# Performance work log

Measured on AMD Instinct MI355X. Metric: run time of the kernel, lower is better.

## Reference

```python
import jax, jax.numpy as jnp
import numpy as np

NEG_SLOPE = 0.2  # PyG GATv2Conv default negative_slope


def _gatv2(h, src, dst, Wl, bl, Wr, br, att, bias, N):
    """GATv2Conv (concat=True). h: [N,Fin]; att: [H,F]; returns [N,H*F]."""
    H, F = att.shape
    xl = (h @ Wl + bl).reshape(N, H, F)  # source transform
    xr = (h @ Wr + br).reshape(N, H, F)  # target transform
    # per-edge GATv2 score: a^T LeakyReLU(xl[src] + xr[dst])
    e = jax.nn.leaky_relu(xl[src] + xr[dst], negative_slope=NEG_SLOPE)  # [E,H,F]
    logits = jnp.einsum('ehf,hf->eh', e, att)  # [E,H]
    # segment softmax over destination nodes (self-loops guarantee nonempty segments)
    m = jax.ops.segment_max(logits, dst, num_segments=N)  # [N,H]
    p = jnp.exp(logits - m[dst])
    s = jax.ops.segment_sum(p, dst, num_segments=N)  # [N,H]
    alpha = p / s[dst]  # [E,H]
    out = jax.ops.segment_sum(alpha[:, :, None] * xl[src], dst, num_segments=N)  # [N,H,F]
    return out.reshape(N, H * F) + bias


def setup_inputs() -> dict:
    key = jax.random.key(0)
    ks = jax.random.split(key, 16)
    N, E = 30000, 480000
    L, D, H, F = 50, 100, 3, 100
    W = D * H  # 300
    sc = 0.1  # keep activations stable through 5 layers
    return {
        'x': jax.random.randint(ks[0], (N,), 0, L),
        'edge_index': jax.random.randint(ks[1], (2, E), 0, N),
        'emb': jax.random.normal(ks[2], (L, D), jnp.float32),
        'Wl0': jax.random.normal(ks[3], (D, W), jnp.float32) * sc,
        'bl0': jnp.zeros((W,), jnp.float32),
        'Wr0': jax.random.normal(ks[4], (D, W), jnp.float32) * sc,
        'br0': jnp.zeros((W,), jnp.float32),
        'att0': jax.random.normal(ks[5], (H, F), jnp.float32) * sc,
        'bias0': jnp.zeros((W,), jnp.float32),
        'Wl': jax.random.normal(ks[6], (4, W, W), jnp.float32) * sc,
        'bl': jnp.zeros((4, W), jnp.float32),
        'Wr': jax.random.normal(ks[7], (4, W, W), jnp.float32) * sc,
        'br': jnp.zeros((4, W), jnp.float32),
        'att': jax.random.normal(ks[8], (4, H, F), jnp.float32) * sc,
        'bias': jnp.zeros((4, W), jnp.float32),
    }


def reference(x, edge_index, emb, Wl0, bl0, Wr0, br0, att0, bias0,
              Wl, bl, Wr, br, att, bias):
    N = x.shape[0]
    loops = jnp.arange(N)
    src = jnp.concatenate([edge_index[0], loops])  # PyG add_self_loops=True
    dst = jnp.concatenate([edge_index[1], loops])
    h = emb[x]  # node_embedding(x).squeeze()
    h = jax.nn.relu(_gatv2(h, src, dst, Wl0, bl0, Wr0, br0, att0, bias0, N))
    for i in range(4):  # remaining num_gnn_layers-1 convs, each followed by ReLU
        h = jax.nn.relu(_gatv2(h, src, dst, Wl[i], bl[i], Wr[i], br[i], att[i], bias[i], N))
    return h  # [N, heads*hidden] = [N, 300]
```

## Files before the change

### kernel.cpp

```cpp
#include <hip/hip_runtime.h>

#define NODES   30000
#define E0N     480000
#define ETOT    510000
#define D0      100
#define WDIM    300
#define NW      600
#define NEG     0.2f

typedef __bf16 bf16x8 __attribute__((ext_vector_type(8)));
typedef float  f32x4  __attribute__((ext_vector_type(4)));

__global__ void gather_emb(const int* __restrict__ x, const float* __restrict__ emb,
                           float* __restrict__ h, int n, int d) {
    int t = blockIdx.x * 256 + threadIdx.x;
    if (t >= n * d) return;
    int i = t / d, k = t - i * d;
    h[t] = emb[x[i] * d + k];
}

__global__ void count_edges(const int* __restrict__ ei, int* __restrict__ counts) {
    int e = blockIdx.x * 256 + threadIdx.x;
    if (e >= ETOT) return;
    int d = (e < E0N) ? ei[E0N + e] : (e - E0N);
    atomicAdd(&counts[d], 1);
}

__global__ __launch_bounds__(1024) void scan_kernel(const int* __restrict__ counts,
                                                    int* __restrict__ offsets, int n) {
    __shared__ int lds[1024];
    const int CH = 32;
    int t = threadIdx.x;
    int base = t * CH;
    int loc[CH];
    int sum = 0;
    #pragma unroll
    for (int i = 0; i < CH; i++) {
        int v = (base + i < n) ? counts[base + i] : 0;
        loc[i] = sum;
        sum += v;
    }
    lds[t] = sum;
    __syncthreads();
    for (int off = 1; off < 1024; off <<= 1) {
        int v = (t >= off) ? lds[t - off] : 0;
        __syncthreads();
        lds[t] += v;
        __syncthreads();
    }
    int ex = (t == 0) ? 0 : lds[t - 1];
    #pragma unroll
    for (int i = 0; i < CH; i++) {
        int idx = base + i;
        if (idx < n) offsets[idx] = ex + loc[i];
    }
    if (t == 0) offsets[n] = lds[1023];
}

__global__ void scatter_edges(const int* __restrict__ ei, const int* __restrict__ offsets,
                              int* __restrict__ cursor, int* __restrict__ csr_src) {
    int e = blockIdx.x * 256 + threadIdx.x;
    if (e >= ETOT) return;
    int s, d;
    if (e < E0N) { s = ei[e]; d = ei[E0N + e]; }
    else         { s = e - E0N; d = s; }
    int pos = offsets[d] + atomicAdd(&cursor[d], 1);
    csr_src[pos] = s;
}

__global__ void make_bfrag(const float* __restrict__ Bl, const float* __restrict__ Br,
                           bf16x8* __restrict__ out, int K, int ksteps) {
    int t = blockIdx.x * 256 + threadIdx.x;
    int total = ksteps * 40 * 64;
    if (t >= total) return;
    int lane = t & 63;
    int n16  = (t >> 6) % 40;
    int s    = t / (64 * 40);
    int c = n16 * 16 + (lane & 15);
    union { bf16x8 v; __bf16 e[8]; } hi, lo;
    #pragma unroll
    for (int j = 0; j < 8; j++) {
        int k = s * 32 + ((lane >> 4) * 8) + j;
        float x = 0.f;
        if (k < K && c < NW)
            x = (c < WDIM) ? Bl[(size_t)k * WDIM + c] : Br[(size_t)k * WDIM + c - WDIM];
        __bf16 h = (__bf16)x;
        hi.e[j] = h;
        lo.e[j] = (__bf16)(x - (float)h);
    }
    size_t base = ((size_t)(s * 40 + n16) * 2) * 64 + lane;
    out[base]      = hi.v;
    out[base + 64] = lo.v;
}

__global__ __launch_bounds__(256) void gemm_mfma(
    const float* __restrict__ A, const bf16x8* __restrict__ Bfrag,
    const float* __restrict__ bl, const float* __restrict__ br,
    float* __restrict__ Cl, float* __restrict__ Cr,
    int M, int K, int ksteps) {

    __shared__ bf16x8 Alds[8][2][64];
    __shared__ bf16x8 Blds[8][2][64];

    int id = blockIdx.x;
    int mb = (id & 7) + 8 * (id / 40);
    int cb = (id >> 3) % 5;
    if (mb >= 235) return;

    int tid  = threadIdx.x;
    int lane = tid & 63;
    int wid  = tid >> 6;
    int wm = wid >> 1, wn = wid & 1;
    int row0 = mb * 128;

    f32x4 acc[4][4] = {};

    for (int s = 0; s < ksteps; s++) {
        int kt = s * 32;
        #pragma unroll
        for (int u0 = 0; u0 < 2; u0++) {
            int u = u0 * 256 + tid;
            int m16  = u >> 6;
            int slot = u & 63;
            int kh = slot >> 4, rl = slot & 15;
            int gr = row0 + m16 * 16 + rl;
            int gc = kt + kh * 8;
            float4 v0 = make_float4(0.f,0.f,0.f,0.f), v1 = v0;
            if (gr < M) {
                const float* ap = A + (size_t)gr * K + gc;
                if (gc + 4 <= K) v0 = *(const float4*)ap;
                if (gc + 8 <= K) v1 = *(const float4*)(ap + 4);
            }
            union { bf16x8 v; __bf16 e[8]; } hi, lo;
            const float* xs0 = (const float*)&v0;
            const float* xs1 = (const float*)&v1;
            #pragma unroll
            for (int j = 0; j < 8; j++) {
                float x = (j < 4) ? xs0[j] : xs1[j - 4];
                __bf16 h = (__bf16)x;
                hi.e[j] = h;
                lo.e[j] = (__bf16)(x - (float)h);
            }
            Alds[m16][0][slot] = hi.v;
            Alds[m16][1][slot] = lo.v;
        }
        {
            const float4* bsrc = (const float4*)(Bfrag + ((size_t)(s * 40 + cb * 8) * 2) * 64);
            float4* bdst = (float4*)&Blds[0][0][0];
            #pragma unroll
            for (int c = 0; c < 4; c++)
                bdst[c * 256 + tid] = bsrc[c * 256 + tid];
        }
        __syncthreads();

        bf16x8 af[4][2], bfr[4][2];
        #pragma unroll
        for (int m = 0; m < 4; m++) {
            af[m][0] = Alds[wm * 4 + m][0][lane];
            af[m][1] = Alds[wm * 4 + m][1][lane];
        }
        #pragma unroll
        for (int n = 0; n < 4; n++) {
            bfr[n][0] = Blds[wn * 4 + n][0][lane];
            bfr[n][1] = Blds[wn * 4 + n][1][lane];
        }
        #pragma unroll
        for (int m = 0; m < 4; m++)
            #pragma unroll
            for (int n = 0; n < 4; n++) {
                acc[m][n] = __builtin_amdgcn_mfma_f32_16x16x32_bf16(af[m][1], bfr[n][1], acc[m][n], 0, 0, 0);
                acc[m][n] = __builtin_amdgcn_mfma_f32_16x16x32_bf16(af[m][1], bfr[n][0], acc[m][n], 0, 0, 0);
                acc[m][n] = __builtin_amdgcn_mfma_f32_16x16x32_bf16(af[m][0], bfr[n][1], acc[m][n], 0, 0, 0);
                acc[m][n] = __builtin_amdgcn_mfma_f32_16x16x32_bf16(af[m][0], bfr[n][0], acc[m][n], 0, 0, 0);
            }
        __syncthreads();
    }

    int r0 = row0 + wm * 64;
    int c0 = cb * 128 + wn * 64;
    #pragma unroll
    for (int m = 0; m < 4; m++)
        #pragma unroll
        for (int n = 0; n < 4; n++) {
            #pragma unroll
            for (int reg = 0; reg < 4; reg++) {
                int gr = r0 + m * 16 + (lane >> 4) * 4 + reg;
                int gc = c0 + n * 16 + (lane & 15);
                if (gr < M && gc < NW) {
                    bool left = gc < WDIM;
                    int cc = left ? gc : gc - WDIM;
                    float v = acc[m][n][reg] + (left ? bl[cc] : br[cc]);
                    (left ? Cl : Cr)[(size_t)gr * WDIM + cc] = v;
                }
            }
        }
}

__global__ __launch_bounds__(256) void gat_edge_agg(
    const float* __restrict__ xl, const float* __restrict__ xr,
    const int* __restrict__ offsets, const int* __restrict__ csr_src,
    const float* __restrict__ att, const float* __restrict__ bias,
    float* __restrict__ hout) {
    int node = (blockIdx.x * 256 + threadIdx.x) >> 6;
    int lane = threadIdx.x & 63;
    if (node >= NODES) return;

    float aw[5], xrv[5];
    #pragma unroll
    for (int j = 0; j < 5; j++) {
        int f = lane + 64 * j;
        aw[j]  = (f < WDIM) ? att[f] : 0.f;
        xrv[j] = xr[(size_t)node * WDIM + ((f < WDIM) ? f : 0)];
    }

    float m0 = -1e38f, m1 = -1e38f, m2 = -1e38f;
    float s0 = 0.f, s1 = 0.f, s2 = 0.f;
    float acc[5] = {};

    int beg = offsets[node], end = offsets[node + 1];
    for (int i = beg; i < end; i += 2) {
        bool act_b = (i + 1) < end;
        int sa = csr_src[i];
        int sb = csr_src[act_b ? i + 1 : i];
        const float* ra = xl + (size_t)sa * WDIM;
        const float* rb = xl + (size_t)sb * WDIM;
        float va[5], vb[5];
        #pragma unroll
        for (int j = 0; j < 5; j++) {
            va[j] = ra[lane + 64 * j];
            vb[j] = rb[lane + 64 * j];
        }
        float pa0 = 0.f, pa1 = 0.f, pa2 = 0.f;
        float pb0 = 0.f, pb1 = 0.f, pb2 = 0.f;
        #pragma unroll
        for (int j = 0; j < 5; j++) {
            int f = lane + 64 * j;
            float ta = va[j] + xrv[j]; ta = fmaxf(ta, NEG * ta);
            float tb = vb[j] + xrv[j]; tb = fmaxf(tb, NEG * tb);
            float qa = ta * aw[j], qb = tb * aw[j];
            if (j == 0)      { pa0 += qa; pb0 += qb; }
            else if (j == 2) { pa1 += qa; pb1 += qb; }
            else if (j == 4) { pa2 += qa; pb2 += qb; }
            else if (j == 1) {
                if (f < 100) { pa0 += qa; pb0 += qb; } else { pa1 += qa; pb1 += qb; }
            } else {
                if (f < 200) { pa1 += qa; pb1 += qb; } else { pa2 += qa; pb2 += qb; }
            }
        }
        pa0 += __shfl_xor(pa0, 1, 64); pa1 += __shfl_xor(pa1, 1, 64); pa2 += __shfl_xor(pa2, 1, 64);
        pb0 += __shfl_xor(pb0, 1, 64); pb1 += __shfl_xor(pb1, 1, 64); pb2 += __shfl_xor(pb2, 1, 64);
        pa0 += __shfl_xor(pa0, 2, 64); pa1 += __shfl_xor(pa1, 2, 64); pa2 += __shfl_xor(pa2, 2, 64);
        pb0 += __shfl_xor(pb0, 2, 64); pb1 += __shfl_xor(pb1, 2, 64); pb2 += __shfl_xor(pb2, 2, 64);
        int r = lane & 3;
        float qa = (r == 1) ? pa1 : ((r == 2) ? pa2 : pa0);
        float qb = (r == 1) ? pb1 : ((r == 2) ? pb2 : pb0);
        qa += __shfl_xor(qa, 4, 64);  qb += __shfl_xor(qb, 4, 64);
        qa += __shfl_xor(qa, 8, 64);  qb += __shfl_xor(qb, 8, 64);
        qa += __shfl_xor(qa, 16, 64); qb += __shfl_xor(qb, 16, 64);
        qa += __shfl_xor(qa, 32, 64); qb += __shfl_xor(qb, 32, 64);
        pa0 = __shfl(qa, 0, 64); pa1 = __shfl(qa, 1, 64); pa2 = __shfl(qa, 2, 64);
        pb0 = __shfl(qb, 0, 64); pb1 = __shfl(qb, 1, 64); pb2 = __shfl(qb, 2, 64);
        if (!act_b) { pb0 = -3e38f; pb1 = -3e38f; pb2 = -3e38f; }

        float hi0 = fmaxf(pa0, pb0), hi1 = fmaxf(pa1, pb1), hi2 = fmaxf(pa2, pb2);
        if (hi0 > m0 + 8.f || hi1 > m1 + 8.f || hi2 > m2 + 8.f) {
            float nm0 = fmaxf(m0, hi0), nm1 = fmaxf(m1, hi1), nm2 = fmaxf(m2, hi2);
            float e0 = __expf(m0 - nm0), e1 = __expf(m1 - nm1), e2 = __expf(m2 - nm2);
            s0 *= e0; s1 *= e1; s2 *= e2;
            #pragma unroll
            for (int j = 0; j < 5; j++) {
                int f = lane + 64 * j;
                float e = (j == 0) ? e0 : (j == 2) ? e1 : (j == 4) ? e2 :
                          (j == 1) ? ((f < 100) ? e0 : e1) : ((f < 200) ? e1 : e2);
                acc[j] *= e;
            }
            m0 = nm0; m1 = nm1; m2 = nm2;
        }
        float ca0 = __expf(pa0 - m0), ca1 = __expf(pa1 - m1), ca2 = __expf(pa2 - m2);
        float cb0 = __expf(pb0 - m0), cb1 = __expf(pb1 - m1), cb2 = __expf(pb2 - m2);
        s0 += ca0 + cb0; s1 += ca1 + cb1; s2 += ca2 + cb2;
        #pragma unroll
        for (int j = 0; j < 5; j++) {
            int f = lane + 64 * j;
            float ca = (j == 0) ? ca0 : (j == 2) ? ca1 : (j == 4) ? ca2 :
                       (j == 1) ? ((f < 100) ? ca0 : ca1) : ((f < 200) ? ca1 : ca2);
            float cb = (j == 0) ? cb0 : (j == 2) ? cb1 : (j == 4) ? cb2 :
                       (j == 1) ? ((f < 100) ? cb0 : cb1) : ((f < 200) ? cb1 : cb2);
            acc[j] = fmaf(ca, va[j], acc[j]);
            acc[j] = fmaf(cb, vb[j], acc[j]);
        }
    }

    float i0 = 1.f / s0, i1 = 1.f / s1, i2 = 1.f / s2;
    #pragma unroll
    for (int j = 0; j < 5; j++) {
        int f = lane + 64 * j;
        if (f < WDIM) {
            float is = (j == 0) ? i0 : (j == 2) ? i1 : (j == 4) ? i2 :
                       (j == 1) ? ((f < 100) ? i0 : i1) : ((f < 200) ? i1 : i2);
            float o = acc[j] * is + bias[f];
            hout[(size_t)node * WDIM + f] = fmaxf(o, 0.f);
        }
    }
}

static inline size_t align256(size_t x) { return (x + 255) & ~(size_t)255; }

extern "C" void kernel_launch(void* const* d_in, const int* in_sizes, int n_in,
                              void* d_out, int out_size, void* d_ws, size_t ws_size,
                              hipStream_t stream) {
    const int*   x     = (const int*)d_in[0];
    const int*   ei    = (const int*)d_in[1];
    const float* emb   = (const float*)d_in[2];
    const float* Wl0   = (const float*)d_in[3];
    const float* bl0   = (const float*)d_in[4];
    const float* Wr0   = (const float*)d_in[5];
    const float* br0   = (const float*)d_in[6];
    const float* att0  = (const float*)d_in[7];
    const float* bias0 = (const float*)d_in[8];
    const float* Wl    = (const float*)d_in[9];
    const float* bl    = (const float*)d_in[10];
    const float* Wr    = (const float*)d_in[11];
    const float* br    = (const float*)d_in[12];
    const float* att   = (const float*)d_in[13];
    const float* bias  = (const float*)d_in[14];

    char* ws = (char*)d_ws;
    size_t off = 0;
    float* h      = (float*)(ws + off); off = align256(off + (size_t)NODES * WDIM * 4);
    float* xlb    = (float*)(ws + off); off = align256(off + (size_t)NODES * WDIM * 4);
    float* xrb    = (float*)(ws + off); off = align256(off + (size_t)NODES * WDIM * 4);
    int* counts   = (int*)(ws + off);   off = align256(off + (size_t)NODES * 4);
    int* cursor   = (int*)(ws + off);   off = align256(off + (size_t)NODES * 4);
    int* offsets  = (int*)(ws + off);   off = align256(off + (size_t)(NODES + 1) * 4);
    int* csr_src  = (int*)(ws + off);   off = align256(off + (size_t)ETOT * 4);
    bf16x8* bfrag = (bf16x8*)(ws + off); off = align256(off + (size_t)10 * 40 * 2 * 64 * 16);

    float* out = (float*)d_out;

    hipMemsetAsync(counts, 0, (size_t)NODES * 4, stream);
    hipMemsetAsync(cursor, 0, (size_t)NODES * 4, stream);
    count_edges<<<(ETOT + 255) / 256, 256, 0, stream>>>(ei, counts);
    scan_kernel<<<1, 1024, 0, stream>>>(counts, offsets, NODES);
    scatter_edges<<<(ETOT + 255) / 256, 256, 0, stream>>>(ei, offsets, cursor, csr_src);

    gather_emb<<<(NODES * D0 + 255) / 256, 256, 0, stream>>>(x, emb, h, NODES, D0);

    int agg_blocks = (NODES + 3) / 4;

    {
        int ks = 4;
        int bf_total = ks * 40 * 64;
        make_bfrag<<<(bf_total + 255) / 256, 256, 0, stream>>>(Wl0, Wr0, bfrag, D0, ks);
        gemm_mfma<<<1200, 256, 0, stream>>>(h, bfrag, bl0, br0, xlb, xrb, NODES, D0, ks);
        gat_edge_agg<<<agg_blocks, 256, 0, stream>>>(xlb, xrb, offsets, csr_src, att0, bias0, h);
    }

    for (int i = 0; i < 4; i++) {
        const float* Wli = Wl + (size_t)i * WDIM * WDIM;
        const float* Wri = Wr + (size_t)i * WDIM * WDIM;
        float* dst = (i == 3) ? out : h;
        int ks = 10;
        int bf_total = ks * 40 * 64;
        make_bfrag<<<(bf_total + 255) / 256, 256, 0, stream>>>(Wli, Wri, bfrag, WDIM, ks);
        gemm_mfma<<<1200, 256, 0, stream>>>(h, bfrag, bl + i * WDIM, br + i * WDIM,
                                            xlb, xrb, NODES, WDIM, ks);
        gat_edge_agg<<<agg_blocks, 256, 0, stream>>>(xlb, xrb, offsets, csr_src,
                                                     att + (size_t)i * WDIM,
                                                     bias + (size_t)i * WDIM, dst);
    }
}
```

Before: 948.8 us.

## Fuse embedding gather into GEMM, drop lo*lo MFMA, lane-parallel softmax state

The first-layer GEMM now reads embedding rows through the node-label index, so the separate gather kernel and its intermediate buffer go away. All five weight fragment buffers are built up front instead of one shared buffer rebuilt before each layer. The GEMM drops the lo*lo term of the split-bf16 product, cutting MFMA work by a quarter at a small precision cost. The edge softmax keeps per-head max and sum in lanes 0-2, uses a wave-wide vote for rescaling, and broadcasts exponentials by shuffle, trading scalar exp work for extra shuffles.

```diff
diff --git a/kernel.cpp b/kernel.cpp
--- a/kernel.cpp
+++ b/kernel.cpp
@@ -10,14 +10,6 @@
 
 typedef __bf16 bf16x8 __attribute__((ext_vector_type(8)));
 typedef float  f32x4  __attribute__((ext_vector_type(4)));
-
-__global__ void gather_emb(const int* __restrict__ x, const float* __restrict__ emb,
-                           float* __restrict__ h, int n, int d) {
-    int t = blockIdx.x * 256 + threadIdx.x;
-    if (t >= n * d) return;
-    int i = t / d, k = t - i * d;
-    h[t] = emb[x[i] * d + k];
-}
 
 __global__ void count_edges(const int* __restrict__ ei, int* __restrict__ counts) {
     int e = blockIdx.x * 256 + threadIdx.x;
@@ -94,7 +86,8 @@
 }
 
 __global__ __launch_bounds__(256) void gemm_mfma(
-    const float* __restrict__ A, const bf16x8* __restrict__ Bfrag,
+    const float* __restrict__ A, const int* __restrict__ xmap, int use_map,
+    const bf16x8* __restrict__ Bfrag,
     const float* __restrict__ bl, const float* __restrict__ br,
     float* __restrict__ Cl, float* __restrict__ Cr,
     int M, int K, int ksteps) {
@@ -127,7 +120,8 @@
             int gc = kt + kh * 8;
             float4 v0 = make_float4(0.f,0.f,0.f,0.f), v1 = v0;
             if (gr < M) {
-                const float* ap = A + (size_t)gr * K + gc;
+                int ar = use_map ? xmap[gr] : gr;
+                const float* ap = A + (size_t)ar * K + gc;
                 if (gc + 4 <= K) v0 = *(const float4*)ap;
                 if (gc + 8 <= K) v1 = *(const float4*)(ap + 4);
             }
@@ -168,7 +162,6 @@
         for (int m = 0; m < 4; m++)
             #pragma unroll
             for (int n = 0; n < 4; n++) {
-                acc[m][n] = __builtin_amdgcn_mfma_f32_16x16x32_bf16(af[m][1], bfr[n][1], acc[m][n], 0, 0, 0);
                 acc[m][n] = __builtin_amdgcn_mfma_f32_16x16x32_bf16(af[m][1], bfr[n][0], acc[m][n], 0, 0, 0);
                 acc[m][n] = __builtin_amdgcn_mfma_f32_16x16x32_bf16(af[m][0], bfr[n][1], acc[m][n], 0, 0, 0);
                 acc[m][n] = __builtin_amdgcn_mfma_f32_16x16x32_bf16(af[m][0], bfr[n][0], acc[m][n], 0, 0, 0);
@@ -204,6 +197,7 @@
     int node = (blockIdx.x * 256 + threadIdx.x) >> 6;
     int lane = threadIdx.x & 63;
     if (node >= NODES) return;
+    int r = lane & 3;
 
     float aw[5], xrv[5];
     #pragma unroll
@@ -213,8 +207,7 @@
         xrv[j] = xr[(size_t)node * WDIM + ((f < WDIM) ? f : 0)];
     }
 
-    float m0 = -1e38f, m1 = -1e38f, m2 = -1e38f;
-    float s0 = 0.f, s1 = 0.f, s2 = 0.f;
+    float mq = -1e38f, sq = 0.f;
     float acc[5] = {};
 
     int beg = offsets[node], end = offsets[node + 1];
@@ -251,22 +244,20 @@
         pb0 += __shfl_xor(pb0, 1, 64); pb1 += __shfl_xor(pb1, 1, 64); pb2 += __shfl_xor(pb2, 1, 64);
         pa0 += __shfl_xor(pa0, 2, 64); pa1 += __shfl_xor(pa1, 2, 64); pa2 += __shfl_xor(pa2, 2, 64);
         pb0 += __shfl_xor(pb0, 2, 64); pb1 += __shfl_xor(pb1, 2, 64); pb2 += __shfl_xor(pb2, 2, 64);
-        int r = lane & 3;
         float qa = (r == 1) ? pa1 : ((r == 2) ? pa2 : pa0);
         float qb = (r == 1) ? pb1 : ((r == 2) ? pb2 : pb0);
         qa += __shfl_xor(qa, 4, 64);  qb += __shfl_xor(qb, 4, 64);
         qa += __shfl_xor(qa, 8, 64);  qb += __shfl_xor(qb, 8, 64);
         qa += __shfl_xor(qa, 16, 64); qb += __shfl_xor(qb, 16, 64);
         qa += __shfl_xor(qa, 32, 64); qb += __shfl_xor(qb, 32, 64);
-        pa0 = __shfl(qa, 0, 64); pa1 = __shfl(qa, 1, 64); pa2 = __shfl(qa, 2, 64);
-        pb0 = __shfl(qb, 0, 64); pb1 = __shfl(qb, 1, 64); pb2 = __shfl(qb, 2, 64);
-        if (!act_b) { pb0 = -3e38f; pb1 = -3e38f; pb2 = -3e38f; }
-
-        float hi0 = fmaxf(pa0, pb0), hi1 = fmaxf(pa1, pb1), hi2 = fmaxf(pa2, pb2);
-        if (hi0 > m0 + 8.f || hi1 > m1 + 8.f || hi2 > m2 + 8.f) {
-            float nm0 = fmaxf(m0, hi0), nm1 = fmaxf(m1, hi1), nm2 = fmaxf(m2, hi2);
-            float e0 = __expf(m0 - nm0), e1 = __expf(m1 - nm1), e2 = __expf(m2 - nm2);
-            s0 *= e0; s1 *= e1; s2 *= e2;
+        if (!act_b) qb = -3e38f;
+
+        float hiq = fmaxf(qa, qb);
+        if (__any(hiq > mq + 8.f)) {
+            float nmq = fmaxf(mq, hiq);
+            float eq = __expf(mq - nmq);
+            sq *= eq;
+            float e0 = __shfl(eq, 0, 64), e1 = __shfl(eq, 1, 64), e2 = __shfl(eq, 2, 64);
             #pragma unroll
             for (int j = 0; j < 5; j++) {
                 int f = lane + 64 * j;
@@ -274,11 +265,12 @@
                           (j == 1) ? ((f < 100) ? e0 : e1) : ((f < 200) ? e1 : e2);
                 acc[j] *= e;
             }
-            m0 = nm0; m1 = nm1; m2 = nm2;
-        }
-        float ca0 = __expf(pa0 - m0), ca1 = __expf(pa1 - m1), ca2 = __expf(pa2 - m2);
-        float cb0 = __expf(pb0 - m0), cb1 = __expf(pb1 - m1), cb2 = __expf(pb2 - m2);
-        s0 += ca0 + cb0; s1 += ca1 + cb1; s2 += ca2 + cb2;
+            mq = nmq;
+        }
+        float cqa = __expf(qa - mq), cqb = __expf(qb - mq);
+        sq += cqa + cqb;
+        float ca0 = __shfl(cqa, 0, 64), ca1 = __shfl(cqa, 1, 64), ca2 = __shfl(cqa, 2, 64);
+        float cb0 = __shfl(cqb, 0, 64), cb1 = __shfl(cqb, 1, 64), cb2 = __shfl(cqb, 2, 64);
         #pragma unroll
         for (int j = 0; j < 5; j++) {
             int f = lane + 64 * j;
@@ -291,7 +283,8 @@
         }
     }
 
-    float i0 = 1.f / s0, i1 = 1.f / s1, i2 = 1.f / s2;
+    float iq = 1.f / sq;
+    float i0 = __shfl(iq, 0, 64), i1 = __shfl(iq, 1, 64), i2 = __shfl(iq, 2, 64);
     #pragma unroll
     for (int j = 0; j < 5; j++) {
         int f = lane + 64 * j;
@@ -334,9 +327,18 @@
     int* cursor   = (int*)(ws + off);   off = align256(off + (size_t)NODES * 4);
     int* offsets  = (int*)(ws + off);   off = align256(off + (size_t)(NODES + 1) * 4);
     int* csr_src  = (int*)(ws + off);   off = align256(off + (size_t)ETOT * 4);
-    bf16x8* bfrag = (bf16x8*)(ws + off); off = align256(off + (size_t)10 * 40 * 2 * 64 * 16);
+    bf16x8* bfrag[5];
+    bfrag[0] = (bf16x8*)(ws + off); off = align256(off + (size_t)4 * 40 * 2 * 64 * 16);
+    for (int i = 1; i < 5; i++) {
+        bfrag[i] = (bf16x8*)(ws + off); off = align256(off + (size_t)10 * 40 * 2 * 64 * 16);
+    }
 
     float* out = (float*)d_out;
+
+    make_bfrag<<<(4 * 40 * 64 + 255) / 256, 256, 0, stream>>>(Wl0, Wr0, bfrag[0], D0, 4);
+    for (int i = 0; i < 4; i++)
+        make_bfrag<<<(10 * 40 * 64 + 255) / 256, 256, 0, stream>>>(
+            Wl + (size_t)i * WDIM * WDIM, Wr + (size_t)i * WDIM * WDIM, bfrag[i + 1], WDIM, 10);
 
     hipMemsetAsync(counts, 0, (size_t)NODES * 4, stream);
     hipMemsetAsync(cursor, 0, (size_t)NODES * 4, stream);
@@ -344,27 +346,15 @@
     scan_kernel<<<1, 1024, 0, stream>>>(counts, offsets, NODES);
     scatter_edges<<<(ETOT + 255) / 256, 256, 0, stream>>>(ei, offsets, cursor, csr_src);
 
-    gather_emb<<<(NODES * D0 + 255) / 256, 256, 0, stream>>>(x, emb, h, NODES, D0);
-
     int agg_blocks = (NODES + 3) / 4;
 
-    {
-        int ks = 4;
-        int bf_total = ks * 40 * 64;
-        make_bfrag<<<(bf_total + 255) / 256, 256, 0, stream>>>(Wl0, Wr0, bfrag, D0, ks);
-        gemm_mfma<<<1200, 256, 0, stream>>>(h, bfrag, bl0, br0, xlb, xrb, NODES, D0, ks);
-        gat_edge_agg<<<agg_blocks, 256, 0, stream>>>(xlb, xrb, offsets, csr_src, att0, bias0, h);
-    }
+    gemm_mfma<<<1200, 256, 0, stream>>>(emb, x, 1, bfrag[0], bl0, br0, xlb, xrb, NODES, D0, 4);
+    gat_edge_agg<<<agg_blocks, 256, 0, stream>>>(xlb, xrb, offsets, csr_src, att0, bias0, h);
 
     for (int i = 0; i < 4; i++) {
-        const float* Wli = Wl + (size_t)i * WDIM * WDIM;
-        const float* Wri = Wr + (size_t)i * WDIM * WDIM;
         float* dst = (i == 3) ? out : h;
-        int ks = 10;
-        int bf_total = ks * 40 * 64;
-        make_bfrag<<<(bf_total + 255) / 256, 256, 0, stream>>>(Wli, Wri, bfrag, WDIM, ks);
-        gemm_mfma<<<1200, 256, 0, stream>>>(h, bfrag, bl + i * WDIM, br + i * WDIM,
-                                            xlb, xrb, NODES, WDIM, ks);
+        gemm_mfma<<<1200, 256, 0, stream>>>(h, nullptr, 0, bfrag[i + 1], bl + i * WDIM, br + i * WDIM,
+                                            xlb, xrb, NODES, WDIM, 10);
         gat_edge_agg<<<agg_blocks, 256, 0, stream>>>(xlb, xrb, offsets, csr_src,
                                                      att + (size_t)i * WDIM,
                                                      bias + (size_t)i * WDIM, dst);
```

Measured after the change: 917.6 us. 1.03x faster.
